# Kernel optimization log

Measured on AMD Instinct MI355X. Metric: run time of the kernel, lower is better.

Reference implementation:

```python
import jax, jax.numpy as jnp
import numpy as np

B, S, E, H = 4, 2048, 1024, 16
D = E // H
EPS = 1e-5


def _ln(x, g, b):
    mu = jnp.mean(x, axis=-1, keepdims=True)
    var = jnp.mean(jnp.square(x - mu), axis=-1, keepdims=True)
    return (x - mu) * jax.lax.rsqrt(var + EPS) * g + b


def setup_inputs() -> dict:
    key = jax.random.key(0)
    ks = jax.random.split(key, 12)
    s = 0.02
    return {
        "inp": jax.random.normal(ks[0], (B, S, E), jnp.float32),
        "ln1_g": jnp.ones((E,), jnp.float32),
        "ln1_b": jnp.zeros((E,), jnp.float32),
        "Wq": jax.random.normal(ks[1], (E, E), jnp.float32) * s,
        "bq": jnp.zeros((E,), jnp.float32),
        "Wk": jax.random.normal(ks[2], (E, E), jnp.float32) * s,
        "bk": jnp.zeros((E,), jnp.float32),
        "Wv": jax.random.normal(ks[3], (E, E), jnp.float32) * s,
        "bv": jnp.zeros((E,), jnp.float32),
        "Wo": jax.random.normal(ks[4], (E, E), jnp.float32) * s,
        "bo": jnp.zeros((E,), jnp.float32),
        "ln2_g": jnp.ones((E,), jnp.float32),
        "ln2_b": jnp.zeros((E,), jnp.float32),
        "W1": jax.random.normal(ks[5], (E, 2 * E), jnp.float32) * s,
        "b1": jnp.zeros((2 * E,), jnp.float32),
        "W2": jax.random.normal(ks[6], (2 * E, E), jnp.float32) * s,
        "b2": jnp.zeros((E,), jnp.float32),
    }


def reference(inp, ln1_g, ln1_b, Wq, bq, Wk, bk, Wv, bv, Wo, bo,
              ln2_g, ln2_b, W1, b1, W2, b2):
    x = _ln(inp, ln1_g, ln1_b)                      # [B,S,E]
    def heads(t):
        return t.reshape(B, S, H, D).transpose(0, 2, 1, 3)  # [B,H,S,D]
    q = heads(x @ Wq + bq)
    k = heads(x @ Wk + bk)
    v = heads(x @ Wv + bv)
    scores = jnp.einsum('bhqd,bhkd->bhqk', q, k) / jnp.sqrt(jnp.float32(D))
    attn = jax.nn.softmax(scores, axis=-1)
    out = jnp.einsum('bhqk,bhkd->bhqd', attn, v)    # [B,H,S,D]
    out = out.transpose(0, 2, 1, 3).reshape(B, S, E)
    out = out @ Wo + bo                             # dropout p=1e-4 -> identity (eval)
    x = x + out                                     # NOTE: residual from normed input (as in source)
    x = _ln(x, ln2_g, ln2_b)
    mlp = jax.nn.gelu(x @ W1 + b1, approximate=False) @ W2 + b2
    return mlp + x
```

## Files before the change

kernel.cpp:

```cpp
#include <hip/hip_runtime.h>
#include <hip/hip_bf16.h>

typedef float f32x4 __attribute__((ext_vector_type(4)));
typedef __bf16 bfv8 __attribute__((ext_vector_type(8)));

constexpr int Bc = 4, Sc = 2048, Ec = 1024, Hc = 16, Dc = 64;
constexpr int Mc = Bc * Sc;

__device__ __forceinline__ uint pkbf(float lo, float hi) {
  uint r;
  asm("v_cvt_pk_bf16_f32 %0, %1, %2" : "=v"(r) : "v"(lo), "v"(hi));
  return r;
}
__device__ __forceinline__ ushort f2bf(float f) {
  __hip_bfloat16 h = __float2bfloat16(f);
  return __builtin_bit_cast(ushort, h);
}
__device__ __forceinline__ float bf2f(ushort u) {
  return __builtin_bit_cast(float, (uint)u << 16);
}

typedef __attribute__((address_space(1))) unsigned int as1_u32;
typedef __attribute__((address_space(3))) unsigned int as3_u32;
__device__ __forceinline__ void cp16(const ushort* g, ushort* l) {
  __builtin_amdgcn_global_load_lds((as1_u32*)g, (as3_u32*)l, 16, 0, 0);
}

__global__ __launch_bounds__(256) void wcvt_all_kernel(
    const float* __restrict__ Wq, const float* __restrict__ Wk,
    const float* __restrict__ Wv, const float* __restrict__ Wo,
    const float* __restrict__ W1, const float* __restrict__ W2,
    ushort* __restrict__ WqkvT, ushort* __restrict__ WoT,
    ushort* __restrict__ W1T, ushort* __restrict__ W2T) {
  int bid = blockIdx.x;
  const float* W;
  ushort* WT;
  int K, N;
  if (bid < 1024) {
    W = Wq; WT = WqkvT; K = 1024; N = 1024;
  } else if (bid < 2048) {
    W = Wk; WT = WqkvT + (size_t)1024 * 1024; K = 1024; N = 1024; bid -= 1024;
  } else if (bid < 3072) {
    W = Wv; WT = WqkvT + (size_t)2 * 1024 * 1024; K = 1024; N = 1024; bid -= 2048;
  } else if (bid < 4096) {
    W = Wo; WT = WoT; K = 1024; N = 1024; bid -= 3072;
  } else if (bid < 6144) {
    W = W1; WT = W1T; K = 1024; N = 2048; bid -= 4096;
  } else {
    W = W2; WT = W2T; K = 2048; N = 1024; bid -= 6144;
  }
  const int nbx = K / 32;
  const int k0 = (bid % nbx) * 32, n0 = (bid / nbx) * 32;
  __shared__ float t[32][33];
  int tx = threadIdx.x, ty = threadIdx.y;
#pragma unroll
  for (int i = 0; i < 32; i += 8)
    t[ty + i][tx] = W[(size_t)(k0 + ty + i) * N + n0 + tx];
  __syncthreads();
#pragma unroll
  for (int i = 0; i < 32; i += 8)
    WT[(size_t)(n0 + ty + i) * K + k0 + tx] = f2bf(t[tx][ty + i]);
}

template <int INF32>
__global__ __launch_bounds__(256) void ln_kernel(const void* in,
                                                 const float* __restrict__ g,
                                                 const float* __restrict__ bb,
                                                 ushort* ob) {
  int row = blockIdx.x;
  int t = threadIdx.x;
  float4 x;
  if constexpr (INF32) {
    x = reinterpret_cast<const float4*>((const float*)in + (size_t)row * Ec)[t];
  } else {
    uint2 u = reinterpret_cast<const uint2*>((const ushort*)in + (size_t)row * Ec)[t];
    x.x = __builtin_bit_cast(float, u.x << 16);
    x.y = __builtin_bit_cast(float, u.x & 0xFFFF0000u);
    x.z = __builtin_bit_cast(float, u.y << 16);
    x.w = __builtin_bit_cast(float, u.y & 0xFFFF0000u);
  }
  float s = x.x + x.y + x.z + x.w;
  float q = x.x * x.x + x.y * x.y + x.z * x.z + x.w * x.w;
#pragma unroll
  for (int o = 32; o > 0; o >>= 1) {
    s += __shfl_down(s, o);
    q += __shfl_down(q, o);
  }
  __shared__ float red[10];
  int wv = t >> 6;
  if ((t & 63) == 0) { red[wv] = s; red[4 + wv] = q; }
  __syncthreads();
  if (t == 0) {
    float S = red[0] + red[1] + red[2] + red[3];
    float Q = red[4] + red[5] + red[6] + red[7];
    float mu = S * (1.f / Ec);
    float var = Q * (1.f / Ec) - mu * mu;
    red[8] = mu;
    red[9] = rsqrtf(var + 1e-5f);
  }
  __syncthreads();
  float mu = red[8], rs = red[9];
  float4 gg = reinterpret_cast<const float4*>(g)[t];
  float4 b4 = reinterpret_cast<const float4*>(bb)[t];
  float4 y;
  y.x = (x.x - mu) * rs * gg.x + b4.x;
  y.y = (x.y - mu) * rs * gg.y + b4.y;
  y.z = (x.z - mu) * rs * gg.z + b4.z;
  y.w = (x.w - mu) * rs * gg.w + b4.w;
  uint2 u;
  u.x = pkbf(y.x, y.y);
  u.y = pkbf(y.z, y.w);
  reinterpret_cast<uint2*>(ob + (size_t)row * Ec)[t] = u;
}

template <int MODE>
__global__ __launch_bounds__(256, 2) void gemm_kernel(
    int M, int N, int K, const ushort* __restrict__ A,
    const ushort* __restrict__ BT, const float* __restrict__ b0,
    const float* __restrict__ b1, const float* __restrict__ b2,
    const ushort* __restrict__ rb, float* outF, ushort* o0, ushort* o1,
    ushort* o2, float qscale) {
  __shared__ __align__(16) ushort As[2][128 * 64];
  __shared__ __align__(16) ushort Bs[2][128 * 64];
  const int tid = threadIdx.x;
  const int lane = tid & 63, wave = tid >> 6;
  const int wr = wave >> 1, wc = wave & 1;
  const int fr = lane & 15, fq = lane >> 4;
  const int nx = gridDim.x;
  int flat = blockIdx.x + nx * blockIdx.y;
  int cpx = (nx * gridDim.y) >> 3;
  int work = (flat & 7) * cpx + (flat >> 3);
  const int n0 = (work % nx) * 128, m0 = (work / nx) * 128;

  f32x4 acc[4][4];
#pragma unroll
  for (int i = 0; i < 4; i++)
#pragma unroll
    for (int j = 0; j < 4; j++) acc[i][j] = f32x4{0.f, 0.f, 0.f, 0.f};

  const int srow = tid >> 3;
  const int sslot = tid & 7;

  auto STAGE = [&](int p, int k0) {
#pragma unroll
    for (int c = 0; c < 4; ++c) {
      int row = c * 32 + srow;
      int scol = (sslot ^ (row & 7)) * 8;
      cp16(A + (size_t)(m0 + row) * K + k0 + scol,
           &As[p][(c * 256 + wave * 64) * 8]);
      cp16(BT + (size_t)(n0 + row) * K + k0 + scol,
           &Bs[p][(c * 256 + wave * 64) * 8]);
    }
  };

  STAGE(0, 0);
  const int nt = K >> 6;
  for (int kt = 0; kt < nt; ++kt) {
    const int p = kt & 1;
    if (kt + 1 < nt) {
      STAGE(p ^ 1, (kt + 1) << 6);
      asm volatile("s_waitcnt vmcnt(8)" ::: "memory");
    } else {
      asm volatile("s_waitcnt vmcnt(0)" ::: "memory");
    }
    __builtin_amdgcn_s_barrier();
#pragma unroll
    for (int kk = 0; kk < 2; ++kk) {
      bfv8 af[4], bf[4];
#pragma unroll
      for (int m = 0; m < 4; m++) {
        int row = wr * 64 + m * 16 + fr;
        af[m] = *reinterpret_cast<const bfv8*>(
            &As[p][row * 64 + (((kk * 4 + fq) ^ (fr & 7)) * 8)]);
      }
#pragma unroll
      for (int n = 0; n < 4; n++) {
        int row = wc * 64 + n * 16 + fr;
        bf[n] = *reinterpret_cast<const bfv8*>(
            &Bs[p][row * 64 + (((kk * 4 + fq) ^ (fr & 7)) * 8)]);
      }
      __builtin_amdgcn_s_setprio(1);
#pragma unroll
      for (int m = 0; m < 4; m++)
#pragma unroll
        for (int n = 0; n < 4; n++)
          acc[m][n] =
              __builtin_amdgcn_mfma_f32_16x16x32_bf16(af[m], bf[n], acc[m][n], 0, 0, 0);
      __builtin_amdgcn_s_setprio(0);
    }
    __builtin_amdgcn_sched_barrier(0);
    __builtin_amdgcn_s_barrier();
  }

#pragma unroll
  for (int m = 0; m < 4; m++) {
#pragma unroll
    for (int n = 0; n < 4; n++) {
      const int row0 = m0 + wr * 64 + m * 16 + fq * 4;
      const int col = n0 + wc * 64 + n * 16 + fr;
      if constexpr (MODE == 0) {
        const int region = col >> 10, c1 = col & (Ec - 1);
        const int b = row0 >> 11, s0 = row0 & (Sc - 1);
        const int h = c1 >> 6, d = c1 & (Dc - 1);
        const float bb = (region == 0 ? b0 : region == 1 ? b1 : b2)[c1];
        if (region == 2) {
          uint2 u;
          u.x = pkbf(acc[m][n][0] + bb, acc[m][n][1] + bb);
          u.y = pkbf(acc[m][n][2] + bb, acc[m][n][3] + bb);
          *reinterpret_cast<uint2*>(
              &o2[(((size_t)b * Hc + h) * Dc + d) * Sc + s0]) = u;
        } else {
          ushort* dst = region ? o1 : o0;
          const float sc = region ? 1.f : qscale;
#pragma unroll
          for (int r = 0; r < 4; r++)
            dst[(((size_t)b * Hc + h) * Sc + s0 + r) * Dc + d] =
                f2bf((acc[m][n][r] + bb) * sc);
        }
      } else {
        const float bb = b0[col];
#pragma unroll
        for (int r = 0; r < 4; r++) {
          int row = row0 + r;
          size_t idx = (size_t)row * N + col;
          float vacc = acc[m][n][r] + bb + bf2f(rb[idx]);
          if constexpr (MODE == 1) {
            o0[idx] = f2bf(vacc);
          } else {
            outF[idx] = vacc;
          }
        }
      }
    }
  }
}

template <int MODE>
__global__ __launch_bounds__(512, 2) void gemm256_kernel(
    int M, int N, int K, const ushort* __restrict__ A,
    const ushort* __restrict__ BT, const float* __restrict__ b0,
    ushort* o0, float qscale) {
  __shared__ __align__(16) ushort As[2][256 * 64];
  __shared__ __align__(16) ushort Bs[2][256 * 64];
  const int tid = threadIdx.x;
  const int lane = tid & 63, wave = tid >> 6;
  const int wr = wave >> 2, wc = wave & 3;
  const int fr = lane & 15, fq = lane >> 4;
  const int nx = gridDim.x;
  int flat = blockIdx.x + nx * blockIdx.y;
  int cpx = (nx * gridDim.y) >> 3;
  int work = (flat & 7) * cpx + (flat >> 3);
  const int n0 = (work % nx) * 256, m0 = (work / nx) * 256;

  f32x4 acc[8][4];
#pragma unroll
  for (int i = 0; i < 8; i++)
#pragma unroll
    for (int j = 0; j < 4; j++) acc[i][j] = f32x4{0.f, 0.f, 0.f, 0.f};

  const int srow = tid >> 3;
  const int sslot = tid & 7;

  auto STAGE = [&](int p, int k0) {
#pragma unroll
    for (int c = 0; c < 4; ++c) {
      int row = c * 64 + srow;
      int scol = (sslot ^ (row & 7)) * 8;
      cp16(A + (size_t)(m0 + row) * K + k0 + scol,
           &As[p][(c * 64 + wave * 8) * 64]);
      cp16(BT + (size_t)(n0 + row) * K + k0 + scol,
           &Bs[p][(c * 64 + wave * 8) * 64]);
    }
  };

  STAGE(0, 0);
  const int nt = K >> 6;
  for (int kt = 0; kt < nt; ++kt) {
    const int p = kt & 1;
    if (kt + 1 < nt) {
      STAGE(p ^ 1, (kt + 1) << 6);
      asm volatile("s_waitcnt vmcnt(8)" ::: "memory");
    } else {
      asm volatile("s_waitcnt vmcnt(0)" ::: "memory");
    }
    __builtin_amdgcn_s_barrier();
#pragma unroll
    for (int kk = 0; kk < 2; ++kk) {
      bfv8 bfr[4];
#pragma unroll
      for (int n = 0; n < 4; ++n) {
        int row = wc * 64 + n * 16 + fr;
        bfr[n] = *reinterpret_cast<const bfv8*>(
            &Bs[p][row * 64 + (((kk * 4 + fq) ^ (row & 7)) * 8)]);
      }
#pragma unroll
      for (int mh = 0; mh < 2; ++mh) {
        bfv8 af[4];
#pragma unroll
        for (int mm = 0; mm < 4; ++mm) {
          int row = wr * 128 + (mh * 4 + mm) * 16 + fr;
          af[mm] = *reinterpret_cast<const bfv8*>(
              &As[p][row * 64 + (((kk * 4 + fq) ^ (row & 7)) * 8)]);
        }
        __builtin_amdgcn_s_setprio(1);
#pragma unroll
        for (int mm = 0; mm < 4; ++mm)
#pragma unroll
          for (int n = 0; n < 4; ++n)
            acc[mh * 4 + mm][n] = __builtin_amdgcn_mfma_f32_16x16x32_bf16(
                af[mm], bfr[n], acc[mh * 4 + mm][n], 0, 0, 0);
        __builtin_amdgcn_s_setprio(0);
        if (!(kk == 1 && mh == 1)) __builtin_amdgcn_s_barrier();
      }
    }
    __builtin_amdgcn_sched_barrier(0);
    __builtin_amdgcn_s_barrier();
  }

#pragma unroll
  for (int m = 0; m < 8; m++) {
#pragma unroll
    for (int n = 0; n < 4; n++) {
      const int row0 = m0 + wr * 128 + m * 16 + fq * 4;
      const int col = n0 + wc * 64 + n * 16 + fr;
      const float bb = b0[col];
#pragma unroll
      for (int r = 0; r < 4; r++) {
        float vacc = acc[m][n][r] + bb;
        vacc = 0.5f * vacc * (1.f + erff(vacc * 0.70710678118f));
        o0[(size_t)(row0 + r) * N + col] = f2bf(vacc);
      }
    }
  }
}

__global__ __launch_bounds__(512) void attn_kernel(const ushort* __restrict__ q,
                                                   const ushort* __restrict__ k,
                                                   const ushort* __restrict__ vt,
                                                   ushort* __restrict__ o) {
  int flat = blockIdx.x;
  int swz = (flat & 7) * 128 + (flat >> 3);
  const int qb = swz & 15;
  const int bh = swz >> 4;
  const int tid = threadIdx.x, lane = tid & 63, wave = tid >> 6;
  const int fr = lane & 15, fq = lane >> 4;
  const size_t base = (size_t)bh * Sc * Dc;
  const int q0 = qb * 128 + wave * 16;

  __shared__ __align__(16) ushort Ks[2][64 * 64];
  __shared__ __align__(16) ushort Vt[2][64 * 64];
  __shared__ __align__(16) ushort Ps[8][16 * 64];

  bfv8 qf0, qf1;
  {
    const ushort* qp = q + base + (size_t)(q0 + fr) * Dc + fq * 8;
    qf0 = *reinterpret_cast<const bfv8*>(qp);
    qf1 = *reinterpret_cast<const bfv8*>(qp + 32);
  }

  const bfv8 ones = __builtin_bit_cast(bfv8, uint4{0x3F803F80u, 0x3F803F80u,
                                                  0x3F803F80u, 0x3F803F80u});

  f32x4 oacc[4];
  f32x4 oaccL;
  oaccL = f32x4{0.f, 0.f, 0.f, 0.f};
#pragma unroll
  for (int d = 0; d < 4; ++d) oacc[d] = f32x4{0.f, 0.f, 0.f, 0.f};

  const int r8 = tid >> 3;
  const int c8 = tid & 7;

  auto STAGE = [&](int p, int key0) {
    int sc = (c8 ^ (r8 & 7)) * 8;
    cp16(k + base + (size_t)(key0 + r8) * Dc + sc, &Ks[p][wave * 512]);
    cp16(vt + base + (size_t)r8 * Sc + key0 + sc, &Vt[p][wave * 512]);
  };

  const int sA = (fq ^ (fr & 7)) * 8;
  const int sB = ((fq + 4) ^ (fr & 7)) * 8;

  const int pswz = 2 * (fr & 7);
  const int pr0 = fr * 64 + ((fq * 2) ^ pswz) * 4;
  const int pr1 = fr * 64 + ((fq * 2 + 8) ^ pswz) * 4;

  STAGE(0, 0);
  constexpr int NT = Sc / 64;
  for (int kt = 0; kt < NT; ++kt) {
    const int p = kt & 1;
    if (kt + 1 < NT) {
      STAGE(p ^ 1, (kt + 1) * 64);
      asm volatile("s_waitcnt vmcnt(2)" ::: "memory");
    } else {
      asm volatile("s_waitcnt vmcnt(0)" ::: "memory");
    }
    __builtin_amdgcn_s_barrier();

    bfv8 kf0[4], kf1[4], vf0[4], vf1[4];
#pragma unroll
    for (int t = 0; t < 4; ++t) {
      int e = (t * 16 + fr) * 64;
      kf0[t] = *reinterpret_cast<const bfv8*>(&Ks[p][e + sA]);
      kf1[t] = *reinterpret_cast<const bfv8*>(&Ks[p][e + sB]);
      vf0[t] = *reinterpret_cast<const bfv8*>(&Vt[p][e + sA]);
      vf1[t] = *reinterpret_cast<const bfv8*>(&Vt[p][e + sB]);
    }

    f32x4 sf[4];
    __builtin_amdgcn_s_setprio(1);
#pragma unroll
    for (int t = 0; t < 4; ++t) {
      sf[t] = f32x4{0.f, 0.f, 0.f, 0.f};
      sf[t] = __builtin_amdgcn_mfma_f32_16x16x32_bf16(kf0[t], qf0, sf[t], 0, 0, 0);
      sf[t] = __builtin_amdgcn_mfma_f32_16x16x32_bf16(kf1[t], qf1, sf[t], 0, 0, 0);
    }
    __builtin_amdgcn_s_setprio(0);
    ushort* pw = &Ps[wave][0];
#pragma unroll
    for (int t = 0; t < 4; ++t) {
      uint2 pu;
      pu.x = pkbf(__builtin_amdgcn_exp2f(sf[t][0]),
                  __builtin_amdgcn_exp2f(sf[t][1]));
      pu.y = pkbf(__builtin_amdgcn_exp2f(sf[t][2]),
                  __builtin_amdgcn_exp2f(sf[t][3]));
      int us = fr * 64 + ((t * 4 + fq) ^ pswz) * 4;
      *reinterpret_cast<uint2*>(&pw[us]) = pu;
    }
    bfv8 pf0 = *reinterpret_cast<const bfv8*>(&pw[pr0]);
    bfv8 pf1 = *reinterpret_cast<const bfv8*>(&pw[pr1]);
    __builtin_amdgcn_s_setprio(1);
#pragma unroll
    for (int d = 0; d < 4; ++d) {
      oacc[d] = __builtin_amdgcn_mfma_f32_16x16x32_bf16(pf0, vf0[d], oacc[d], 0, 0, 0);
      oacc[d] = __builtin_amdgcn_mfma_f32_16x16x32_bf16(pf1, vf1[d], oacc[d], 0, 0, 0);
    }
    oaccL = __builtin_amdgcn_mfma_f32_16x16x32_bf16(pf0, ones, oaccL, 0, 0, 0);
    oaccL = __builtin_amdgcn_mfma_f32_16x16x32_bf16(pf1, ones, oaccL, 0, 0, 0);
    __builtin_amdgcn_s_setprio(0);

    __builtin_amdgcn_sched_barrier(0);
    __builtin_amdgcn_s_barrier();
  }

  const int b = bh >> 4, h = bh & 15;
  float linv[4];
#pragma unroll
  for (int r = 0; r < 4; ++r) linv[r] = 1.f / oaccL[r];
#pragma unroll
  for (int d = 0; d < 4; ++d)
#pragma unroll
    for (int r = 0; r < 4; ++r) {
      int sIdx = q0 + fq * 4 + r;
      o[((size_t)(b * Sc + sIdx)) * Ec + h * 64 + d * 16 + fr] =
          f2bf(oacc[d][r] * linv[r]);
    }
}

extern "C" void kernel_launch(void* const* d_in, const int* in_sizes, int n_in,
                              void* d_out, int out_size, void* d_ws, size_t ws_size,
                              hipStream_t stream) {
  const float* inp = (const float*)d_in[0];
  const float* ln1g = (const float*)d_in[1];
  const float* ln1b = (const float*)d_in[2];
  const float* Wq = (const float*)d_in[3];
  const float* bq = (const float*)d_in[4];
  const float* Wk = (const float*)d_in[5];
  const float* bk = (const float*)d_in[6];
  const float* Wv = (const float*)d_in[7];
  const float* bv = (const float*)d_in[8];
  const float* Wo = (const float*)d_in[9];
  const float* bo = (const float*)d_in[10];
  const float* ln2g = (const float*)d_in[11];
  const float* ln2b = (const float*)d_in[12];
  const float* W1 = (const float*)d_in[13];
  const float* b1 = (const float*)d_in[14];
  const float* W2 = (const float*)d_in[15];
  const float* b2 = (const float*)d_in[16];

  char* wsb = (char*)d_ws;
  size_t off = 0;
  auto alloc = [&](size_t bytes) {
    char* p = wsb + off;
    off += (bytes + 255) & ~(size_t)255;
    return p;
  };
  ushort* xb = (ushort*)alloc((size_t)Mc * Ec * 2);
  ushort* x2b = (ushort*)alloc((size_t)Mc * Ec * 2);
  ushort* x3b = (ushort*)alloc((size_t)Mc * Ec * 2);
  ushort* qbuf = (ushort*)alloc((size_t)Mc * Ec * 2);
  ushort* kbuf = (ushort*)alloc((size_t)Mc * Ec * 2);
  ushort* vtbuf = (ushort*)alloc((size_t)Mc * Ec * 2);
  ushort* abuf = (ushort*)alloc((size_t)Mc * Ec * 2);
  ushort* h1 = (ushort*)alloc((size_t)Mc * 2 * Ec * 2);
  ushort* WqkvT = (ushort*)alloc((size_t)3 * Ec * Ec * 2);
  ushort* WoT = (ushort*)alloc((size_t)Ec * Ec * 2);
  ushort* W1T = (ushort*)alloc((size_t)Ec * 2 * Ec * 2);
  ushort* W2T = (ushort*)alloc((size_t)Ec * 2 * Ec * 2);
  (void)in_sizes; (void)n_in; (void)out_size; (void)ws_size;

  wcvt_all_kernel<<<8192, dim3(32, 8), 0, stream>>>(Wq, Wk, Wv, Wo, W1, W2,
                                                    WqkvT, WoT, W1T, W2T);

  ln_kernel<1><<<Mc, 256, 0, stream>>>(inp, ln1g, ln1b, xb);

  gemm_kernel<0><<<dim3(3 * Ec / 128, Mc / 128), 256, 0, stream>>>(
      Mc, 3 * Ec, Ec, xb, WqkvT, bq, bk, bv, nullptr, nullptr, qbuf, kbuf,
      vtbuf, 0.18033688f);

  attn_kernel<<<Bc * Hc * (Sc / 128), 512, 0, stream>>>(qbuf, kbuf, vtbuf, abuf);

  gemm_kernel<1><<<dim3(Ec / 128, Mc / 128), 256, 0, stream>>>(
      Mc, Ec, Ec, abuf, WoT, bo, nullptr, nullptr, xb, nullptr, x2b, nullptr,
      nullptr, 1.f);

  ln_kernel<0><<<Mc, 256, 0, stream>>>(x2b, ln2g, ln2b, x3b);

  gemm256_kernel<2><<<dim3(2 * Ec / 256, Mc / 256), 512, 0, stream>>>(
      Mc, 2 * Ec, Ec, x3b, W1T, b1, h1, 1.f);

  gemm_kernel<3><<<dim3(Ec / 128, Mc / 128), 256, 0, stream>>>(
      Mc, Ec, 2 * Ec, h1, W2T, b2, nullptr, nullptr, x3b, (float*)d_out,
      nullptr, nullptr, nullptr, 1.f);
}
```

Baseline: 309.1 us.

## Stage 128-key K/V tiles per iteration in attention kernel

Doubles the key tile staged into shared memory per loop iteration from 64 to 128 keys, halving the number of barrier-synchronised iterations. Each iteration now processes two 64-key halves in sequence, with a wider 128-column swizzle for the transposed V buffer and vmcnt adjusted for four outstanding copies. The aim is to amortise barrier and wait overhead over more MFMA work, at the cost of doubled LDS use (about 80KB per block), which may reduce occupancy.

```diff
diff --git a/kernel.cpp b/kernel.cpp
--- a/kernel.cpp
+++ b/kernel.cpp
@@ -347,8 +347,8 @@
   const size_t base = (size_t)bh * Sc * Dc;
   const int q0 = qb * 128 + wave * 16;
 
-  __shared__ __align__(16) ushort Ks[2][64 * 64];
-  __shared__ __align__(16) ushort Vt[2][64 * 64];
+  __shared__ __align__(16) ushort Ks[2][128 * 64];
+  __shared__ __align__(16) ushort Vt[2][64 * 128];
   __shared__ __align__(16) ushort Ps[8][16 * 64];
 
   bfv8 qf0, qf1;
@@ -367,75 +367,96 @@
 #pragma unroll
   for (int d = 0; d < 4; ++d) oacc[d] = f32x4{0.f, 0.f, 0.f, 0.f};
 
-  const int r8 = tid >> 3;
-  const int c8 = tid & 7;
+  const int rk = tid >> 3;
+  const int ck = tid & 7;
+  const int rv = tid >> 4;
+  const int cv = tid & 15;
 
   auto STAGE = [&](int p, int key0) {
-    int sc = (c8 ^ (r8 & 7)) * 8;
-    cp16(k + base + (size_t)(key0 + r8) * Dc + sc, &Ks[p][wave * 512]);
-    cp16(vt + base + (size_t)r8 * Sc + key0 + sc, &Vt[p][wave * 512]);
+#pragma unroll
+    for (int i = 0; i < 2; ++i) {
+      int krow = i * 64 + rk;
+      int skc = (ck ^ (krow & 7)) * 8;
+      cp16(k + base + (size_t)(key0 + krow) * Dc + skc,
+           &Ks[p][(i * 64 + wave * 8) * 64]);
+    }
+#pragma unroll
+    for (int i = 0; i < 2; ++i) {
+      int vrow = i * 32 + rv;
+      int svc = (cv ^ (vrow & 15)) * 8;
+      cp16(vt + base + (size_t)vrow * Sc + key0 + svc,
+           &Vt[p][(i * 32 + wave * 4) * 128]);
+    }
   };
-
-  const int sA = (fq ^ (fr & 7)) * 8;
-  const int sB = ((fq + 4) ^ (fr & 7)) * 8;
 
   const int pswz = 2 * (fr & 7);
   const int pr0 = fr * 64 + ((fq * 2) ^ pswz) * 4;
   const int pr1 = fr * 64 + ((fq * 2 + 8) ^ pswz) * 4;
 
   STAGE(0, 0);
-  constexpr int NT = Sc / 64;
+  constexpr int NT = Sc / 128;
   for (int kt = 0; kt < NT; ++kt) {
     const int p = kt & 1;
     if (kt + 1 < NT) {
-      STAGE(p ^ 1, (kt + 1) * 64);
-      asm volatile("s_waitcnt vmcnt(2)" ::: "memory");
+      STAGE(p ^ 1, (kt + 1) * 128);
+      asm volatile("s_waitcnt vmcnt(4)" ::: "memory");
     } else {
       asm volatile("s_waitcnt vmcnt(0)" ::: "memory");
     }
     __builtin_amdgcn_s_barrier();
 
-    bfv8 kf0[4], kf1[4], vf0[4], vf1[4];
-#pragma unroll
-    for (int t = 0; t < 4; ++t) {
-      int e = (t * 16 + fr) * 64;
-      kf0[t] = *reinterpret_cast<const bfv8*>(&Ks[p][e + sA]);
-      kf1[t] = *reinterpret_cast<const bfv8*>(&Ks[p][e + sB]);
-      vf0[t] = *reinterpret_cast<const bfv8*>(&Vt[p][e + sA]);
-      vf1[t] = *reinterpret_cast<const bfv8*>(&Vt[p][e + sB]);
-    }
-
-    f32x4 sf[4];
-    __builtin_amdgcn_s_setprio(1);
-#pragma unroll
-    for (int t = 0; t < 4; ++t) {
-      sf[t] = f32x4{0.f, 0.f, 0.f, 0.f};
-      sf[t] = __builtin_amdgcn_mfma_f32_16x16x32_bf16(kf0[t], qf0, sf[t], 0, 0, 0);
-      sf[t] = __builtin_amdgcn_mfma_f32_16x16x32_bf16(kf1[t], qf1, sf[t], 0, 0, 0);
-    }
-    __builtin_amdgcn_s_setprio(0);
-    ushort* pw = &Ps[wave][0];
-#pragma unroll
-    for (int t = 0; t < 4; ++t) {
-      uint2 pu;
-      pu.x = pkbf(__builtin_amdgcn_exp2f(sf[t][0]),
-                  __builtin_amdgcn_exp2f(sf[t][1]));
-      pu.y = pkbf(__builtin_amdgcn_exp2f(sf[t][2]),
-                  __builtin_amdgcn_exp2f(sf[t][3]));
-      int us = fr * 64 + ((t * 4 + fq) ^ pswz) * 4;
-      *reinterpret_cast<uint2*>(&pw[us]) = pu;
-    }
-    bfv8 pf0 = *reinterpret_cast<const bfv8*>(&pw[pr0]);
-    bfv8 pf1 = *reinterpret_cast<const bfv8*>(&pw[pr1]);
-    __builtin_amdgcn_s_setprio(1);
-#pragma unroll
-    for (int d = 0; d < 4; ++d) {
-      oacc[d] = __builtin_amdgcn_mfma_f32_16x16x32_bf16(pf0, vf0[d], oacc[d], 0, 0, 0);
-      oacc[d] = __builtin_amdgcn_mfma_f32_16x16x32_bf16(pf1, vf1[d], oacc[d], 0, 0, 0);
-    }
-    oaccL = __builtin_amdgcn_mfma_f32_16x16x32_bf16(pf0, ones, oaccL, 0, 0, 0);
-    oaccL = __builtin_amdgcn_mfma_f32_16x16x32_bf16(pf1, ones, oaccL, 0, 0, 0);
-    __builtin_amdgcn_s_setprio(0);
+#pragma unroll
+    for (int h = 0; h < 2; ++h) {
+      f32x4 sf[4];
+      bfv8 kf0[4], kf1[4];
+#pragma unroll
+      for (int t = 0; t < 4; ++t) {
+        int row = h * 64 + t * 16 + fr;
+        kf0[t] = *reinterpret_cast<const bfv8*>(
+            &Ks[p][row * 64 + ((fq ^ (row & 7)) * 8)]);
+        kf1[t] = *reinterpret_cast<const bfv8*>(
+            &Ks[p][row * 64 + (((4 + fq) ^ (row & 7)) * 8)]);
+      }
+      __builtin_amdgcn_s_setprio(1);
+#pragma unroll
+      for (int t = 0; t < 4; ++t) {
+        sf[t] = f32x4{0.f, 0.f, 0.f, 0.f};
+        sf[t] = __builtin_amdgcn_mfma_f32_16x16x32_bf16(kf0[t], qf0, sf[t], 0, 0, 0);
+        sf[t] = __builtin_amdgcn_mfma_f32_16x16x32_bf16(kf1[t], qf1, sf[t], 0, 0, 0);
+      }
+      __builtin_amdgcn_s_setprio(0);
+      ushort* pw = &Ps[wave][0];
+#pragma unroll
+      for (int t = 0; t < 4; ++t) {
+        uint2 pu;
+        pu.x = pkbf(__builtin_amdgcn_exp2f(sf[t][0]),
+                    __builtin_amdgcn_exp2f(sf[t][1]));
+        pu.y = pkbf(__builtin_amdgcn_exp2f(sf[t][2]),
+                    __builtin_amdgcn_exp2f(sf[t][3]));
+        int us = fr * 64 + ((t * 4 + fq) ^ pswz) * 4;
+        *reinterpret_cast<uint2*>(&pw[us]) = pu;
+      }
+      bfv8 pf0 = *reinterpret_cast<const bfv8*>(&pw[pr0]);
+      bfv8 pf1 = *reinterpret_cast<const bfv8*>(&pw[pr1]);
+      bfv8 vf0[4], vf1[4];
+#pragma unroll
+      for (int t = 0; t < 4; ++t) {
+        int row = t * 16 + fr;
+        vf0[t] = *reinterpret_cast<const bfv8*>(
+            &Vt[p][row * 128 + (((h * 8 + fq) ^ (row & 15)) * 8)]);
+        vf1[t] = *reinterpret_cast<const bfv8*>(
+            &Vt[p][row * 128 + (((h * 8 + 4 + fq) ^ (row & 15)) * 8)]);
+      }
+      __builtin_amdgcn_s_setprio(1);
+#pragma unroll
+      for (int d = 0; d < 4; ++d) {
+        oacc[d] = __builtin_amdgcn_mfma_f32_16x16x32_bf16(pf0, vf0[d], oacc[d], 0, 0, 0);
+        oacc[d] = __builtin_amdgcn_mfma_f32_16x16x32_bf16(pf1, vf1[d], oacc[d], 0, 0, 0);
+      }
+      oaccL = __builtin_amdgcn_mfma_f32_16x16x32_bf16(pf0, ones, oaccL, 0, 0, 0);
+      oaccL = __builtin_amdgcn_mfma_f32_16x16x32_bf16(pf1, ones, oaccL, 0, 0, 0);
+      __builtin_amdgcn_s_setprio(0);
+    }
 
     __builtin_amdgcn_sched_barrier(0);
     __builtin_amdgcn_s_barrier();
```

Result: no change. 306.3 us (-0.9%).
